# Performance work log

Hardware: AMD Instinct MI355X
Metric: run time of the kernel (lower is better)

The kernel has to match this reference:

```python
import jax, jax.numpy as jnp
import numpy as np
import math

OMEGA_0 = 30.0
LAYER_SIZES = [3, 256, 256, 256, 256, 3]
N_POINTS = 524288


def _siren_params(key):
    """SIREN initialization matching the original module."""
    keys = jax.random.split(key, len(LAYER_SIZES) - 1)
    params = {}
    for i in range(len(LAYER_SIZES) - 1):
        in_dim, out_dim = LAYER_SIZES[i], LAYER_SIZES[i + 1]
        k = keys[i]
        bound = (1.0 / in_dim) if i == 0 else (math.sqrt(6.0 / in_dim) / OMEGA_0)
        W = jax.random.uniform(k, (out_dim, in_dim), minval=-bound, maxval=bound, dtype=jnp.float32)
        b = jax.random.uniform(k, (out_dim,), minval=-1e-6, maxval=1e-6, dtype=jnp.float32)
        params[f"W{i}"] = W
        params[f"b{i}"] = b
    return params


def setup_inputs() -> dict:
    key = jax.random.key(0)
    kx, kp = jax.random.split(key)
    # coordinates in [-1, 1], typical SIREN input domain
    x = jax.random.uniform(kx, (N_POINTS, 3), minval=-1.0, maxval=1.0, dtype=jnp.float32)
    inp = {"x": x}
    inp.update(_siren_params(kp))
    return inp


def reference(x, W0, b0, W1, b1, W2, b2, W3, b3, W4, b4):
    # First layer: sin(omega_0 * (W0 @ x + b0)), batched over rows of x.
    h = jnp.sin(OMEGA_0 * (jnp.einsum("ni,oi->no", x, W0) + b0))
    # Hidden layers: sin(W @ h + b)
    h = jnp.sin(jnp.einsum("ni,oi->no", h, W1) + b1)
    h = jnp.sin(jnp.einsum("ni,oi->no", h, W2) + b2)
    h = jnp.sin(jnp.einsum("ni,oi->no", h, W3) + b3)
    # Final layer: linear, no activation.
    out = jnp.einsum("ni,oi->no", h, W4) + b4
    return out
```

## Files before the change

### kernel.cpp

```cpp
#include <hip/hip_runtime.h>
#include <stdint.h>


typedef float    f32x4 __attribute__((ext_vector_type(4)));
typedef short    s16x8 __attribute__((ext_vector_type(8)));
typedef uint32_t u32x2 __attribute__((ext_vector_type(2)));
typedef uint32_t u32x4 __attribute__((ext_vector_type(4)));

#define INV2PI 0.15915494309189535f
#define L0SCALE 4.774648292756860f
#define W4OFF 196608

__device__ __forceinline__ uint16_t f32_to_bf16(float f) {
    uint32_t u = __builtin_bit_cast(uint32_t, f);
    u += 0x7FFFu + ((u >> 16) & 1u);
    return (uint16_t)(u >> 16);
}
__device__ __forceinline__ uint32_t pack_bf16x2(float lo, float hi) {
#if __has_builtin(__builtin_amdgcn_cvt_pk_bf16_f32)
    auto v = __builtin_amdgcn_cvt_pk_bf16_f32(lo, hi);
    return __builtin_bit_cast(uint32_t, v);
#else
    uint32_t a = __builtin_bit_cast(uint32_t, lo);
    uint32_t b = __builtin_bit_cast(uint32_t, hi);
    a += 0x7FFFu + ((a >> 16) & 1u);
    b += 0x7FFFu + ((b >> 16) & 1u);
    return (a >> 16) | (b & 0xFFFF0000u);
#endif
}
__device__ __forceinline__ float sin_rev(float r) {
    return __builtin_amdgcn_sinf(r);
}

__global__ void convert_weights(const float* __restrict__ W1,
                                const float* __restrict__ W2,
                                const float* __restrict__ W3,
                                const float* __restrict__ W4,
                                uint16_t* __restrict__ wsb) {
    int tid = blockIdx.x * blockDim.x + threadIdx.x;
    if (tid < 196608) {
        int l = tid >> 16;
        int r = tid & 65535;
        int c = r >> 8;
        int k = r & 255;
        const float* W = (l == 0) ? W1 : (l == 1) ? W2 : W3;
        int kc = k >> 5, q = (k >> 3) & 3, j = k & 7;
        wsb[(((l * 8 + kc) * 16 + (c >> 4)) * 64 + q * 16 + (c & 15)) * 8 + j] =
            f32_to_bf16(W[c * 256 + k] * INV2PI);
    } else if (tid < 200704) {
        int e = tid - 196608;
        int kc = e >> 9, lane = (e >> 3) & 63, j = e & 7;
        int n16 = lane & 15, q = lane >> 4;
        float v = (n16 < 3) ? W4[n16 * 256 + kc * 32 + q * 8 + j] : 0.0f;
        wsb[W4OFF + (kc * 64 + lane) * 8 + j] = f32_to_bf16(v);
    }
}

__global__ __launch_bounds__(256, 3) void siren_main(
    const float* __restrict__ x,
    const float* __restrict__ W0, const float* __restrict__ b0,
    const float* __restrict__ b1, const float* __restrict__ b2,
    const float* __restrict__ b3,
    const float* __restrict__ b4,
    const uint16_t* __restrict__ Wb,
    float* __restrict__ out)
{
    __shared__ uint16_t h_lds[2048 * 8];

    const int tid  = threadIdx.x;
    const int lane = tid & 63;
    const int wid  = tid >> 6;
    const int n16  = lane & 15;
    const int q    = lane >> 4;
    const int p0   = blockIdx.x * 64;

    {
        float xv[4][3];
        #pragma unroll
        for (int rt = 0; rt < 4; ++rt) {
            const float* xp = x + (p0 + rt * 16 + n16) * 3;
            xv[rt][0] = xp[0]; xv[rt][1] = xp[1]; xv[rt][2] = xp[2];
        }
        #pragma unroll
        for (int oo = 0; oo < 2; ++oo) {
            const int octet = wid * 8 + oo * 4 + q;
            const float* w0r = W0 + octet * 24;
            float wv[24];
            #pragma unroll
            for (int i = 0; i < 24; ++i) wv[i] = w0r[i] * L0SCALE;
            float bb[8];
            #pragma unroll
            for (int i = 0; i < 8; ++i) bb[i] = b0[octet * 8 + i] * L0SCALE;
            const int kc0 = octet >> 2, q0 = octet & 3;
            #pragma unroll
            for (int rt = 0; rt < 4; ++rt) {
                u32x4 pk;
                #pragma unroll
                for (int j2 = 0; j2 < 4; ++j2) {
                    float za = wv[(2*j2  )*3+0] * xv[rt][0] +
                               wv[(2*j2  )*3+1] * xv[rt][1] +
                               wv[(2*j2  )*3+2] * xv[rt][2] + bb[2*j2];
                    float zb = wv[(2*j2+1)*3+0] * xv[rt][0] +
                               wv[(2*j2+1)*3+1] * xv[rt][1] +
                               wv[(2*j2+1)*3+2] * xv[rt][2] + bb[2*j2+1];
                    pk[j2] = pack_bf16x2(sin_rev(za), sin_rev(zb));
                }
                *(u32x4*)&h_lds[((kc0 * 4 + rt) * 64 + q0 * 16 + n16) * 8] = pk;
            }
        }
    }
    __syncthreads();

    #pragma unroll
    for (int l = 0; l < 3; ++l) {
        const uint16_t* wsl = Wb + l * 65536;
        const float* bl = (l == 0) ? b1 : (l == 1) ? b2 : b3;

        s16x8 Wbuf[2][2][4];
        #pragma unroll
        for (int kc2 = 0; kc2 < 2; ++kc2)
            #pragma unroll
            for (int t = 0; t < 4; ++t)
                Wbuf[0][kc2][t] = *(const s16x8*)(wsl + ((kc2 * 16 + wid * 4 + t) * 64 + lane) * 8);

        f32x4 acc[4][4];
        #pragma unroll
        for (int t = 0; t < 4; ++t) {
            f32x4 bv = *(const f32x4*)&bl[wid * 64 + t * 16 + q * 4];
            bv *= INV2PI;
            #pragma unroll
            for (int pt = 0; pt < 4; ++pt) acc[t][pt] = bv;
        }

        #pragma unroll
        for (int kp = 0; kp < 4; ++kp) {
            const int cur = kp & 1, nxt = cur ^ 1;
            if (kp < 3) {
                #pragma unroll
                for (int kc2 = 0; kc2 < 2; ++kc2)
                    #pragma unroll
                    for (int t = 0; t < 4; ++t)
                        Wbuf[nxt][kc2][t] = *(const s16x8*)(wsl +
                            (((kp * 2 + 2 + kc2) * 16 + wid * 4 + t) * 64 + lane) * 8);
            }
            #pragma unroll
            for (int kc2 = 0; kc2 < 2; ++kc2) {
                const int kc = kp * 2 + kc2;
                s16x8 hf[4];
                #pragma unroll
                for (int pt = 0; pt < 4; ++pt)
                    hf[pt] = *(const s16x8*)&h_lds[((kc * 4 + pt) * 64 + lane) * 8];
                #pragma unroll
                for (int t = 0; t < 4; ++t)
                    #pragma unroll
                    for (int pt = 0; pt < 4; ++pt)
                        acc[t][pt] = __builtin_amdgcn_mfma_f32_16x16x32_bf16(
                            Wbuf[cur][kc2][t], hf[pt], acc[t][pt], 0, 0, 0);
            }
        }
        __syncthreads();

        uint32_t* hw = (uint32_t*)h_lds;
        #pragma unroll
        for (int t = 0; t < 4; ++t) {
            const int kcp = wid * 2 + (t >> 1);
            const int qp  = (t * 2 + (q >> 1)) & 3;
            #pragma unroll
            for (int pt = 0; pt < 4; ++pt) {
                float s0 = sin_rev(acc[t][pt][0]);
                float s1 = sin_rev(acc[t][pt][1]);
                float s2 = sin_rev(acc[t][pt][2]);
                float s3 = sin_rev(acc[t][pt][3]);
                int base = ((kcp * 4 + pt) * 64 + qp * 16 + n16) * 4 + (q & 1) * 2;
                u32x2 w2 = { pack_bf16x2(s0, s1), pack_bf16x2(s2, s3) };
                *(u32x2*)&hw[base] = w2;
            }
        }
        __syncthreads();
    }

    {
        float bb4 = (n16 < 3) ? b4[n16] : 0.0f;
        f32x4 accF = { bb4, bb4, bb4, bb4 };
        #pragma unroll
        for (int kc = 0; kc < 8; ++kc) {
            s16x8 w4f = *(const s16x8*)(Wb + W4OFF + (kc * 64 + lane) * 8);
            s16x8 af  = *(const s16x8*)&h_lds[((kc * 4 + wid) * 64 + lane) * 8];
            accF = __builtin_amdgcn_mfma_f32_16x16x32_bf16(af, w4f, accF, 0, 0, 0);
        }
        if (n16 < 3) {
            #pragma unroll
            for (int r = 0; r < 4; ++r)
                out[(p0 + wid * 16 + q * 4 + r) * 3 + n16] = accF[r];
        }
    }
}

extern "C" void kernel_launch(void* const* d_in, const int* in_sizes, int n_in,
                              void* d_out, int out_size, void* d_ws, size_t ws_size,
                              hipStream_t stream) {
    const float* x  = (const float*)d_in[0];
    const float* W0 = (const float*)d_in[1];
    const float* b0 = (const float*)d_in[2];
    const float* W1 = (const float*)d_in[3];
    const float* b1 = (const float*)d_in[4];
    const float* W2 = (const float*)d_in[5];
    const float* b2 = (const float*)d_in[6];
    const float* W3 = (const float*)d_in[7];
    const float* b3 = (const float*)d_in[8];
    const float* W4 = (const float*)d_in[9];
    const float* b4 = (const float*)d_in[10];
    float* outp     = (float*)d_out;
    uint16_t* wsb   = (uint16_t*)d_ws;

    hipLaunchKernelGGL(convert_weights, dim3(784), dim3(256), 0, stream,
                       W1, W2, W3, W4, wsb);
    hipLaunchKernelGGL(siren_main, dim3(8192), dim3(256), 0, stream,
                       x, W0, b0, b1, b2, b3, b4, wsb, outp);
}
```

Before: 299.6 us.

## Switch hidden layers to 32x32x16 MFMA with new weight and LDS layouts

Hidden-layer GEMMs now use 32x32x16 bf16 MFMA tiles instead of 16x16x32. The weight and activation LDS layouts are reorganized to match, and the first weight tile of each layer is prefetched during the previous layer or the layer-0 compute. The aim is fewer LDS fragment loads per MFMA and higher MFMA throughput per instruction, plus hidden weight-load latency across layer boundaries. The trade-off is larger accumulators and possible register pressure or LDS bank conflicts.

```diff
diff --git a/kernel.cpp b/kernel.cpp
--- a/kernel.cpp
+++ b/kernel.cpp
@@ -2,10 +2,11 @@
 #include <stdint.h>
 
 
-typedef float    f32x4 __attribute__((ext_vector_type(4)));
-typedef short    s16x8 __attribute__((ext_vector_type(8)));
-typedef uint32_t u32x2 __attribute__((ext_vector_type(2)));
-typedef uint32_t u32x4 __attribute__((ext_vector_type(4)));
+typedef float    f32x4  __attribute__((ext_vector_type(4)));
+typedef float    f32x16 __attribute__((ext_vector_type(16)));
+typedef short    s16x8  __attribute__((ext_vector_type(8)));
+typedef uint32_t u32x2  __attribute__((ext_vector_type(2)));
+typedef uint32_t u32x4  __attribute__((ext_vector_type(4)));
 
 #define INV2PI 0.15915494309189535f
 #define L0SCALE 4.774648292756860f
@@ -44,15 +45,17 @@
         int c = r >> 8;
         int k = r & 255;
         const float* W = (l == 0) ? W1 : (l == 1) ? W2 : W3;
-        int kc = k >> 5, q = (k >> 3) & 3, j = k & 7;
-        wsb[(((l * 8 + kc) * 16 + (c >> 4)) * 64 + q * 16 + (c & 15)) * 8 + j] =
+        int kc16 = k >> 4, cb = c >> 5;
+        int lane = (c & 31) | (((k >> 3) & 1) << 5);
+        int j = k & 7;
+        wsb[(((l * 16 + kc16) * 8 + cb) * 64 + lane) * 8 + j] =
             f32_to_bf16(W[c * 256 + k] * INV2PI);
     } else if (tid < 200704) {
         int e = tid - 196608;
-        int kc = e >> 9, lane = (e >> 3) & 63, j = e & 7;
+        int kk = e >> 9, lane = (e >> 3) & 63, j = e & 7;
         int n16 = lane & 15, q = lane >> 4;
-        float v = (n16 < 3) ? W4[n16 * 256 + kc * 32 + q * 8 + j] : 0.0f;
-        wsb[W4OFF + (kc * 64 + lane) * 8 + j] = f32_to_bf16(v);
+        float v = (n16 < 3) ? W4[n16 * 256 + kk * 32 + q * 8 + j] : 0.0f;
+        wsb[W4OFF + (kk * 64 + lane) * 8 + j] = f32_to_bf16(v);
     }
 }
 
@@ -72,7 +75,17 @@
     const int wid  = tid >> 6;
     const int n16  = lane & 15;
     const int q    = lane >> 4;
+    const int lam  = lane & 31;
+    const int hi   = lane >> 5;
     const int p0   = blockIdx.x * 64;
+
+    s16x8 Wbuf[2][2][2];
+    #pragma unroll
+    for (int kc2 = 0; kc2 < 2; ++kc2)
+        #pragma unroll
+        for (int t = 0; t < 2; ++t)
+            Wbuf[0][kc2][t] = *(const s16x8*)(Wb +
+                ((kc2 * 8 + wid * 2 + t) * 64 + lane) * 8);
 
     {
         float xv[4][3];
@@ -91,7 +104,6 @@
             float bb[8];
             #pragma unroll
             for (int i = 0; i < 8; ++i) bb[i] = b0[octet * 8 + i] * L0SCALE;
-            const int kc0 = octet >> 2, q0 = octet & 3;
             #pragma unroll
             for (int rt = 0; rt < 4; ++rt) {
                 u32x4 pk;
@@ -105,7 +117,10 @@
                                wv[(2*j2+1)*3+2] * xv[rt][2] + bb[2*j2+1];
                     pk[j2] = pack_bf16x2(sin_rev(za), sin_rev(zb));
                 }
-                *(u32x4*)&h_lds[((kc0 * 4 + rt) * 64 + q0 * 16 + n16) * 8] = pk;
+                const int pt = rt * 16 + n16;
+                const int u = ((octet >> 1) * 2 + (pt >> 5)) * 64
+                            + (octet & 1) * 32 + (pt & 31);
+                *(u32x4*)&h_lds[u * 8] = pk;
             }
         }
     }
@@ -113,69 +128,73 @@
 
     #pragma unroll
     for (int l = 0; l < 3; ++l) {
-        const uint16_t* wsl = Wb + l * 65536;
         const float* bl = (l == 0) ? b1 : (l == 1) ? b2 : b3;
 
-        s16x8 Wbuf[2][2][4];
-        #pragma unroll
-        for (int kc2 = 0; kc2 < 2; ++kc2)
-            #pragma unroll
-            for (int t = 0; t < 4; ++t)
-                Wbuf[0][kc2][t] = *(const s16x8*)(wsl + ((kc2 * 16 + wid * 4 + t) * 64 + lane) * 8);
-
-        f32x4 acc[4][4];
-        #pragma unroll
-        for (int t = 0; t < 4; ++t) {
-            f32x4 bv = *(const f32x4*)&bl[wid * 64 + t * 16 + q * 4];
-            bv *= INV2PI;
-            #pragma unroll
-            for (int pt = 0; pt < 4; ++pt) acc[t][pt] = bv;
-        }
-
-        #pragma unroll
-        for (int kp = 0; kp < 4; ++kp) {
+        f32x16 acc[2][2];
+        #pragma unroll
+        for (int t = 0; t < 2; ++t)
+            #pragma unroll
+            for (int g = 0; g < 4; ++g) {
+                f32x4 bv = *(const f32x4*)&bl[wid * 64 + t * 32 + g * 8 + hi * 4];
+                bv *= INV2PI;
+                #pragma unroll
+                for (int i = 0; i < 4; ++i) {
+                    acc[t][0][g * 4 + i] = bv[i];
+                    acc[t][1][g * 4 + i] = bv[i];
+                }
+            }
+
+        #pragma unroll
+        for (int kp = 0; kp < 8; ++kp) {
             const int cur = kp & 1, nxt = cur ^ 1;
-            if (kp < 3) {
+            if (kp < 7) {
                 #pragma unroll
                 for (int kc2 = 0; kc2 < 2; ++kc2)
                     #pragma unroll
-                    for (int t = 0; t < 4; ++t)
-                        Wbuf[nxt][kc2][t] = *(const s16x8*)(wsl +
-                            (((kp * 2 + 2 + kc2) * 16 + wid * 4 + t) * 64 + lane) * 8);
+                    for (int t = 0; t < 2; ++t)
+                        Wbuf[nxt][kc2][t] = *(const s16x8*)(Wb +
+                            (((l * 16 + kp * 2 + 2 + kc2) * 8 + wid * 2 + t) * 64 + lane) * 8);
+            } else if (l < 2) {
+                #pragma unroll
+                for (int kc2 = 0; kc2 < 2; ++kc2)
+                    #pragma unroll
+                    for (int t = 0; t < 2; ++t)
+                        Wbuf[nxt][kc2][t] = *(const s16x8*)(Wb +
+                            ((((l + 1) * 16 + kc2) * 8 + wid * 2 + t) * 64 + lane) * 8);
             }
             #pragma unroll
             for (int kc2 = 0; kc2 < 2; ++kc2) {
-                const int kc = kp * 2 + kc2;
-                s16x8 hf[4];
-                #pragma unroll
-                for (int pt = 0; pt < 4; ++pt)
-                    hf[pt] = *(const s16x8*)&h_lds[((kc * 4 + pt) * 64 + lane) * 8];
-                #pragma unroll
-                for (int t = 0; t < 4; ++t)
+                const int kc16 = kp * 2 + kc2;
+                s16x8 hf[2];
+                #pragma unroll
+                for (int s = 0; s < 2; ++s)
+                    hf[s] = *(const s16x8*)&h_lds[((kc16 * 2 + s) * 64 + lane) * 8];
+                #pragma unroll
+                for (int t = 0; t < 2; ++t)
                     #pragma unroll
-                    for (int pt = 0; pt < 4; ++pt)
-                        acc[t][pt] = __builtin_amdgcn_mfma_f32_16x16x32_bf16(
-                            Wbuf[cur][kc2][t], hf[pt], acc[t][pt], 0, 0, 0);
+                    for (int s = 0; s < 2; ++s)
+                        acc[t][s] = __builtin_amdgcn_mfma_f32_32x32x16_bf16(
+                            Wbuf[cur][kc2][t], hf[s], acc[t][s], 0, 0, 0);
             }
         }
         __syncthreads();
 
         uint32_t* hw = (uint32_t*)h_lds;
         #pragma unroll
-        for (int t = 0; t < 4; ++t) {
-            const int kcp = wid * 2 + (t >> 1);
-            const int qp  = (t * 2 + (q >> 1)) & 3;
-            #pragma unroll
-            for (int pt = 0; pt < 4; ++pt) {
-                float s0 = sin_rev(acc[t][pt][0]);
-                float s1 = sin_rev(acc[t][pt][1]);
-                float s2 = sin_rev(acc[t][pt][2]);
-                float s3 = sin_rev(acc[t][pt][3]);
-                int base = ((kcp * 4 + pt) * 64 + qp * 16 + n16) * 4 + (q & 1) * 2;
-                u32x2 w2 = { pack_bf16x2(s0, s1), pack_bf16x2(s2, s3) };
-                *(u32x2*)&hw[base] = w2;
-            }
-        }
+        for (int t = 0; t < 2; ++t)
+            #pragma unroll
+            for (int s = 0; s < 2; ++s)
+                #pragma unroll
+                for (int g = 0; g < 4; ++g) {
+                    float v0 = sin_rev(acc[t][s][g * 4 + 0]);
+                    float v1 = sin_rev(acc[t][s][g * 4 + 1]);
+                    float v2 = sin_rev(acc[t][s][g * 4 + 2]);
+                    float v3 = sin_rev(acc[t][s][g * 4 + 3]);
+                    const int kc16p = wid * 4 + t * 2 + (g >> 1);
+                    const int u = (kc16p * 2 + s) * 64 + (g & 1) * 32 + lam;
+                    u32x2 w2 = { pack_bf16x2(v0, v1), pack_bf16x2(v2, v3) };
+                    *(u32x2*)&hw[u * 4 + hi * 2] = w2;
+                }
         __syncthreads();
     }
 
@@ -183,9 +202,11 @@
         float bb4 = (n16 < 3) ? b4[n16] : 0.0f;
         f32x4 accF = { bb4, bb4, bb4, bb4 };
         #pragma unroll
-        for (int kc = 0; kc < 8; ++kc) {
-            s16x8 w4f = *(const s16x8*)(Wb + W4OFF + (kc * 64 + lane) * 8);
-            s16x8 af  = *(const s16x8*)&h_lds[((kc * 4 + wid) * 64 + lane) * 8];
+        for (int kk = 0; kk < 8; ++kk) {
+            s16x8 w4f = *(const s16x8*)(Wb + W4OFF + (kk * 64 + lane) * 8);
+            const int u = ((kk * 2 + (q >> 1)) * 2 + (wid >> 1)) * 64
+                        + (q & 1) * 32 + (wid & 1) * 16 + n16;
+            s16x8 af = *(const s16x8*)&h_lds[u * 8];
             accF = __builtin_amdgcn_mfma_f32_16x16x32_bf16(af, w4f, accF, 0, 0, 0);
         }
         if (n16 < 3) {
```

New measurement: 307.2 us. 2.5% more time.
